# Kernel optimization log

Measured on AMD Instinct MI355X. Metric: run time of the kernel, lower is better.

Reference implementation:

```python
import jax, jax.numpy as jnp
import numpy as np

N_HEAD = 32
N_KV_HEAD = 8
HD = 64  # head dim
N_EMBD = 2048
B, T = 2, 2048
ROPE_THETA = 10000.0


def _apply_rope(x, cos, sin):
    # x: [B, T, H, HD]; cos/sin: [T, HD//2]. Interleaved complex pairs (even, odd),
    # matching torch.view_as_complex on x.reshape(..., -1, 2).
    x0 = x[..., 0::2]
    x1 = x[..., 1::2]
    c = cos[None, :, None, :]
    s = sin[None, :, None, :]
    o0 = x0 * c - x1 * s
    o1 = x0 * s + x1 * c
    return jnp.stack([o0, o1], axis=-1).reshape(x.shape)


def setup_inputs() -> dict:
    key = jax.random.key(0)
    k1, k2, k3 = jax.random.split(key, 3)
    x = jax.random.normal(k1, (B, T, N_EMBD), dtype=jnp.float32)
    Wqkv = jax.random.normal(k2, ((N_HEAD + 2 * N_KV_HEAD) * HD, N_EMBD), dtype=jnp.float32) * 0.02
    Wproj = jax.random.normal(k3, (N_EMBD, N_EMBD), dtype=jnp.float32) * 0.02
    # precompute_freqs_cis as in llm.c (llama path)
    freqs = 1.0 / (ROPE_THETA ** (np.arange(0, HD, 2, dtype=np.float32) / HD))
    ang = np.outer(np.arange(T, dtype=np.float32), freqs)  # [T, HD//2]
    freqs_cos = jnp.asarray(np.cos(ang), dtype=jnp.float32)
    freqs_sin = jnp.asarray(np.sin(ang), dtype=jnp.float32)
    return {"x": x, "Wqkv": Wqkv, "Wproj": Wproj,
            "freqs_cos": freqs_cos, "freqs_sin": freqs_sin, "start_pos": -1}


def reference(x, Wqkv, Wproj, freqs_cos, freqs_sin, start_pos):
    Bx, Tx, C = x.shape
    n_rep = N_HEAD // N_KV_HEAD
    qkv = x @ Wqkv.T  # [B, T, (H + 2*KV)*HD]
    q = qkv[..., : N_HEAD * HD].reshape(Bx, Tx, N_HEAD, HD)
    k = qkv[..., N_HEAD * HD: (N_HEAD + N_KV_HEAD) * HD].reshape(Bx, Tx, N_KV_HEAD, HD)
    v = qkv[..., (N_HEAD + N_KV_HEAD) * HD:].reshape(Bx, Tx, N_KV_HEAD, HD)
    # RoPE on q, k
    q = _apply_rope(q, freqs_cos, freqs_sin)
    k = _apply_rope(k, freqs_cos, freqs_sin)
    # start_pos < 0: training path, no KV cache. GQA repeat of kv heads.
    k = jnp.repeat(k, n_rep, axis=2)  # [B, T, H, HD]
    v = jnp.repeat(v, n_rep, axis=2)
    q = q.transpose(0, 2, 1, 3)  # [B, H, T, HD]
    k = k.transpose(0, 2, 1, 3)
    v = v.transpose(0, 2, 1, 3)
    scale = 1.0 / np.sqrt(HD).astype(np.float32)
    scores = jnp.einsum("bhtd,bhsd->bhts", q, k) * scale  # [B, H, T, T]
    causal = jnp.tril(jnp.ones((Tx, Tx), dtype=bool))
    scores = jnp.where(causal[None, None, :, :], scores, -jnp.inf)
    att = jax.nn.softmax(scores.astype(jnp.float32), axis=-1).astype(q.dtype)
    y = jnp.einsum("bhts,bhsd->bhtd", att, v)
    y = y.transpose(0, 2, 1, 3).reshape(Bx, Tx, C)
    return y @ Wproj.T
```

## Files before the change

kernel.cpp:

```cpp
#include <hip/hip_runtime.h>
#include <hip/hip_bf16.h>
#include <cstdint>

#define NH   32
#define NKV  8
#define HD   64
#define CE   2048
#define BB   2
#define TT   2048
#define QKVD 3072
#define MM   (BB*TT)

typedef float  f32x4  __attribute__((ext_vector_type(4)));
typedef float  f32x16 __attribute__((ext_vector_type(16)));
typedef short  s16x8  __attribute__((ext_vector_type(8)));
typedef unsigned short u16;

#define AS1 __attribute__((address_space(1)))
#define AS3 __attribute__((address_space(3)))
#define GLDS16(src, dst) __builtin_amdgcn_global_load_lds( \
    (const AS1 uint32_t*)(src), (AS3 uint32_t*)(dst), 16, 0, 0)

static __device__ __forceinline__ float bf2f(u16 u) {
    union { uint32_t u; float f; } v; v.u = ((uint32_t)u) << 16; return v.f;
}
static __device__ __forceinline__ u16 f2bf(float f) {
    union { float f; uint32_t u; } v; v.f = f;
    uint32_t r = v.u + 0x7fffu + ((v.u >> 16) & 1u);
    return (u16)(r >> 16);
}
static __device__ __forceinline__ uint32_t cvtpk(float lo, float hi) {
    uint32_t r;
    asm("v_cvt_pk_bf16_f32 %0, %1, %2" : "=v"(r) : "v"(lo), "v"(hi));
    return r;
}
static __device__ __forceinline__ void plswap(uint32_t &a, uint32_t &b) {
    asm volatile("v_permlane32_swap_b32 %0, %1" : "+v"(a), "+v"(b));
}

__global__ void k_f32_to_bf16(const float* __restrict__ in, uint32_t* __restrict__ out, int n8) {
    int i = blockIdx.x * blockDim.x + threadIdx.x;
    if (i >= n8) return;
    const float4* p = reinterpret_cast<const float4*>(in) + (size_t)i * 2;
    float4 a = p[0], b = p[1];
    uint4 o;
    o.x = cvtpk(a.x, a.y); o.y = cvtpk(a.z, a.w);
    o.z = cvtpk(b.x, b.y); o.w = cvtpk(b.z, b.w);
    *reinterpret_cast<uint4*>(out + (size_t)i * 4) = o;
}

__global__ __launch_bounds__(256) void k_gemm_qkv(const u16* __restrict__ A,
                                                  const u16* __restrict__ Bm,
                                                  u16* __restrict__ Qb,
                                                  u16* __restrict__ Kb,
                                                  u16* __restrict__ Vt,
                                                  const float* __restrict__ fcos,
                                                  const float* __restrict__ fsin) {
    __shared__ u16 As[128 * 32];
    __shared__ u16 Bs[128 * 32];
    const int K = CE;
    const int c  = blockIdx.x + 24 * blockIdx.y;
    const int nc = (c & 7) * 96 + (c >> 3);
    const int m0 = (nc / 24) * 128;
    const int n0 = (nc % 24) * 128;

    const int tid  = threadIdx.x;
    const int w    = tid >> 6;
    const int lane = tid & 63;
    const int lr   = lane & 15, lg = lane >> 4;
    const int wm   = (w >> 1) * 64, wn = (w & 1) * 64;

    const int o0 = w * 2048 + lane * 16, o1 = o0 + 1024;
    const int ar0 = o0 >> 6, ar1 = o1 >> 6;
    const int ac0 = (o0 & 63) >> 1, ac1 = (o1 & 63) >> 1;
    const size_t aof0 = (size_t)(m0 + ar0) * K + ac0;
    const size_t aof1 = (size_t)(m0 + ar1) * K + ac1;
    const size_t bof0 = (size_t)(n0 + ar0) * K + ac0;
    const size_t bof1 = (size_t)(n0 + ar1) * K + ac1;
    u16* dA0 = &As[w * 1024];       u16* dA1 = &As[w * 1024 + 512];
    u16* dB0 = &Bs[w * 1024];       u16* dB1 = &Bs[w * 1024 + 512];

    f32x4 acc[4][4] = {};

    for (int k0 = 0; k0 < K; k0 += 32) {
        GLDS16(A  + aof0 + k0, dA0);
        GLDS16(A  + aof1 + k0, dA1);
        GLDS16(Bm + bof0 + k0, dB0);
        GLDS16(Bm + bof1 + k0, dB1);
        __syncthreads();
        s16x8 af[4], bf[4];
        #pragma unroll
        for (int i = 0; i < 4; ++i)
            af[i] = *reinterpret_cast<const s16x8*>(&As[(wm + i * 16 + lr) * 32 + lg * 8]);
        #pragma unroll
        for (int j = 0; j < 4; ++j)
            bf[j] = *reinterpret_cast<const s16x8*>(&Bs[(wn + j * 16 + lr) * 32 + lg * 8]);
        #pragma unroll
        for (int i = 0; i < 4; ++i)
            #pragma unroll
            for (int j = 0; j < 4; ++j)
                acc[i][j] = __builtin_amdgcn_mfma_f32_16x16x32_bf16(af[i], bf[j], acc[i][j], 0, 0, 0);
        __syncthreads();
    }

    const float QS = 0.18033688011112042f;
    const int bb = m0 / TT;
    const int tb = m0 - bb * TT + wm;
    #pragma unroll
    for (int i = 0; i < 4; ++i) {
        const int t0 = tb + i * 16 + lg * 4;
        #pragma unroll
        for (int j = 0; j < 4; ++j) {
            const int n = n0 + wn + j * 16 + lr;
            if (n0 < NH * HD) {
                const int hh = n >> 6, d = n & 63;
                #pragma unroll
                for (int r = 0; r < 4; ++r) {
                    const int t = t0 + r;
                    const float cc = fcos[t * 32 + (d >> 1)];
                    const float ss = fsin[t * 32 + (d >> 1)];
                    float v = acc[i][j][r];
                    float p = __shfl_xor(v, 1, 64);
                    float o = ((lr & 1) ? (p * ss + v * cc) : (v * cc - p * ss)) * QS;
                    float po = __shfl_xor(o, 1, 64);
                    if (!(lr & 1))
                        *reinterpret_cast<uint32_t*>(Qb + ((size_t)((bb * NH + hh) * TT + t)) * HD + d) = cvtpk(o, po);
                }
            } else if (n0 < (NH + NKV) * HD) {
                const int fk = n - NH * HD;
                const int hh = fk >> 6, d = fk & 63;
                #pragma unroll
                for (int r = 0; r < 4; ++r) {
                    const int t = t0 + r;
                    const float cc = fcos[t * 32 + (d >> 1)];
                    const float ss = fsin[t * 32 + (d >> 1)];
                    float v = acc[i][j][r];
                    float p = __shfl_xor(v, 1, 64);
                    float o = (lr & 1) ? (p * ss + v * cc) : (v * cc - p * ss);
                    float po = __shfl_xor(o, 1, 64);
                    if (!(lr & 1))
                        *reinterpret_cast<uint32_t*>(Kb + ((size_t)((bb * NKV + hh) * TT + t)) * HD + d) = cvtpk(o, po);
                }
            } else {
                const int fv = n - (NH + NKV) * HD;
                const int vh = fv >> 6, d = fv & 63;
                uint2 st;
                st.x = cvtpk(acc[i][j][0], acc[i][j][1]);
                st.y = cvtpk(acc[i][j][2], acc[i][j][3]);
                *reinterpret_cast<uint2*>(Vt + ((size_t)(bb * NKV + vh) * HD + d) * TT + t0) = st;
            }
        }
    }
}

__global__ __launch_bounds__(256) void k_gemm_bt(const u16* __restrict__ A,
                                                 const u16* __restrict__ Bm,
                                                 float* __restrict__ Cout,
                                                 int M, int N, int K) {
    __shared__ u16 As[128 * 32];
    __shared__ u16 Bs[128 * 32];
    const int c  = blockIdx.x + 16 * blockIdx.y;
    const int nc = (c & 7) * 64 + (c >> 3);
    const int m0 = (nc >> 4) * 128;
    const int n0 = (nc & 15) * 128;

    const int tid  = threadIdx.x;
    const int w    = tid >> 6;
    const int lane = tid & 63;
    const int lr   = lane & 15, lg = lane >> 4;
    const int wm   = (w >> 1) * 64, wn = (w & 1) * 64;

    const int o0 = w * 2048 + lane * 16, o1 = o0 + 1024;
    const int ar0 = o0 >> 6, ar1 = o1 >> 6;
    const int ac0 = (o0 & 63) >> 1, ac1 = (o1 & 63) >> 1;
    const size_t aof0 = (size_t)(m0 + ar0) * K + ac0;
    const size_t aof1 = (size_t)(m0 + ar1) * K + ac1;
    const size_t bof0 = (size_t)(n0 + ar0) * K + ac0;
    const size_t bof1 = (size_t)(n0 + ar1) * K + ac1;
    u16* dA0 = &As[w * 1024];       u16* dA1 = &As[w * 1024 + 512];
    u16* dB0 = &Bs[w * 1024];       u16* dB1 = &Bs[w * 1024 + 512];

    f32x4 acc[4][4] = {};

    for (int k0 = 0; k0 < K; k0 += 32) {
        GLDS16(A  + aof0 + k0, dA0);
        GLDS16(A  + aof1 + k0, dA1);
        GLDS16(Bm + bof0 + k0, dB0);
        GLDS16(Bm + bof1 + k0, dB1);
        __syncthreads();
        s16x8 af[4], bf[4];
        #pragma unroll
        for (int i = 0; i < 4; ++i)
            af[i] = *reinterpret_cast<const s16x8*>(&As[(wm + i * 16 + lr) * 32 + lg * 8]);
        #pragma unroll
        for (int j = 0; j < 4; ++j)
            bf[j] = *reinterpret_cast<const s16x8*>(&Bs[(wn + j * 16 + lr) * 32 + lg * 8]);
        #pragma unroll
        for (int i = 0; i < 4; ++i)
            #pragma unroll
            for (int j = 0; j < 4; ++j)
                acc[i][j] = __builtin_amdgcn_mfma_f32_16x16x32_bf16(af[i], bf[j], acc[i][j], 0, 0, 0);
        __syncthreads();
    }

    #pragma unroll
    for (int i = 0; i < 4; ++i)
        #pragma unroll
        for (int j = 0; j < 4; ++j)
            #pragma unroll
            for (int r = 0; r < 4; ++r) {
                int m = m0 + wm + i * 16 + lg * 4 + r;
                int n = n0 + wn + j * 16 + lr;
                Cout[(size_t)m * N + n] = acc[i][j][r];
            }
}

__global__ __launch_bounds__(512) void k_attn(const u16* __restrict__ Q,
                                              const u16* __restrict__ Kb,
                                              const u16* __restrict__ Vt,
                                              u16* __restrict__ Y) {
    __shared__ u16 Ks[2][4096];
    __shared__ u16 Vs[2][4096];

    const int tid = threadIdx.x;
    const int w = tid >> 6, lane = tid & 63;
    const int wv = w & 3, half = w >> 2;
    const int ql = lane & 31, hi = lane >> 5;
    const int hi16 = hi << 4;
    const int b = blockIdx.z, h = blockIdx.y, kvh = h >> 2;
    const int u = blockIdx.x;

    const int j1 = b ? (8 + u) : (15 - u);
    const int j2 = b ? (7 - u) : u;
    const int jq = half ? j2 : j1;
    const int q0w  = jq * 128 + wv * 32;
    const int nt   = 2 * j1 + 2;
    const int tmxw = (q0w + 31) >> 6;
    const int qabs = q0w + ql;

    const u16* qbase = Q  + ((size_t)(b * NH  + h  ) * TT) * HD;
    const u16* kbase = Kb + ((size_t)(b * NKV + kvh) * TT) * HD;
    const u16* vbase = Vt + ((size_t)(b * NKV + kvh) * HD) * TT;

    const int o0 = w * 1024 + lane * 16;
    const int r0 = o0 >> 7;
    const int c0 = (o0 & 127) ^ ((r0 & 7) << 4);
    const size_t kof0 = (size_t)r0 * HD + (c0 >> 1);
    const size_t vof0 = (size_t)r0 * TT + (c0 >> 1);

    const char* KsB = (const char*)&Ks[0][0];
    const char* VsB = (const char*)&Vs[0][0];
    const int krb0 = (0 * 32 + ql) * 128, ksz0 = ((0 * 32 + ql) & 7) << 4;
    const int krb1 = (1 * 32 + ql) * 128, ksz1 = ((1 * 32 + ql) & 7) << 4;

    s16x8 qf[4];
    #pragma unroll
    for (int ds = 0; ds < 4; ++ds)
        qf[ds] = *reinterpret_cast<const s16x8*>(qbase + (size_t)qabs * HD + ds * 16 + 8 * hi);
    asm volatile("s_waitcnt vmcnt(0)" ::: "memory");

    GLDS16(kbase + kof0, &Ks[0][w * 512]);
    GLDS16(vbase + vof0, &Vs[0][w * 512]);

    float mrow = -1e30f, lrowp = 0.f;
    f32x16 oT0 = {}, oT1 = {};

    for (int t = 0; t < nt; ++t) {
        const int cur = t & 1;
        const int kv0 = t * 64;
        if (t + 1 < nt) {
            GLDS16(kbase + (size_t)(kv0 + 64) * HD + kof0, &Ks[cur ^ 1][w * 512]);
            GLDS16(vbase + (kv0 + 64) + vof0, &Vs[cur ^ 1][w * 512]);
            asm volatile("s_waitcnt vmcnt(2)" ::: "memory");
        } else {
            asm volatile("s_waitcnt vmcnt(0)" ::: "memory");
        }
        __builtin_amdgcn_s_barrier();
        __builtin_amdgcn_sched_barrier(0);

        if (t <= tmxw) {
            const int bufo = cur * 8192;

            f32x16 sc0 = {}, sc1 = {};
            __builtin_amdgcn_s_setprio(1);
            #pragma unroll
            for (int ds = 0; ds < 4; ++ds) {
                s16x8 k0 = *reinterpret_cast<const s16x8*>(KsB + bufo + krb0 + (((ds << 5) | hi16) ^ ksz0));
                s16x8 k1 = *reinterpret_cast<const s16x8*>(KsB + bufo + krb1 + (((ds << 5) | hi16) ^ ksz1));
                sc0 = __builtin_amdgcn_mfma_f32_32x32x16_bf16(k0, qf[ds], sc0, 0, 0, 0);
                sc1 = __builtin_amdgcn_mfma_f32_32x32x16_bf16(k1, qf[ds], sc1, 0, 0, 0);
            }
            __builtin_amdgcn_s_setprio(0);

            float p0[16], p1[16];
            #pragma unroll
            for (int r = 0; r < 16; ++r) { p0[r] = sc0[r]; p1[r] = sc1[r]; }

            if (t == tmxw) {
                const int dq = qabs - kv0 - 4 * hi;
                #pragma unroll
                for (int r = 0; r < 16; ++r) {
                    const int kr = (r & 3) + 8 * (r >> 2);
                    p0[r] = (kr      <= dq) ? p0[r] : -1e30f;
                    p1[r] = (kr + 32 <= dq) ? p1[r] : -1e30f;
                }
            }

            float tmax = fmaxf(p0[0], p1[0]);
            #pragma unroll
            for (int r = 1; r < 16; ++r) tmax = fmaxf(fmaxf(tmax, p0[r]), p1[r]);
            if (__any(tmax > mrow + 8.f)) {
                float tf = fmaxf(tmax, __shfl_xor(tmax, 32, 64));
                float mn = fmaxf(mrow, tf);
                float alpha = __builtin_amdgcn_exp2f(mrow - mn);
                mrow = mn;
                lrowp *= alpha;
                #pragma unroll
                for (int r = 0; r < 16; ++r) { oT0[r] *= alpha; oT1[r] *= alpha; }
            }

            float sum = 0.f;
            #pragma unroll
            for (int r = 0; r < 16; ++r) {
                p0[r] = __builtin_amdgcn_exp2f(p0[r] - mrow);
                p1[r] = __builtin_amdgcn_exp2f(p1[r] - mrow);
                sum += p0[r] + p1[r];
            }
            lrowp += sum;

            __builtin_amdgcn_s_setprio(1);
            #pragma unroll
            for (int ks = 0; ks < 2; ++ks) {
                uint32_t a0 = cvtpk(p0[ks * 8 + 0], p0[ks * 8 + 1]);
                uint32_t b0 = cvtpk(p0[ks * 8 + 4], p0[ks * 8 + 5]);
                plswap(a0, b0);
                uint32_t a1 = cvtpk(p0[ks * 8 + 2], p0[ks * 8 + 3]);
                uint32_t b1 = cvtpk(p0[ks * 8 + 6], p0[ks * 8 + 7]);
                plswap(a1, b1);
                union { uint32_t d[4]; s16x8 v; } pb;
                pb.d[0] = a0; pb.d[1] = a1; pb.d[2] = b0; pb.d[3] = b1;
                const int colb = (0 << 6) | (ks << 5) | hi16;
                s16x8 v0 = *reinterpret_cast<const s16x8*>(VsB + bufo + krb0 + (colb ^ ksz0));
                s16x8 v1 = *reinterpret_cast<const s16x8*>(VsB + bufo + krb1 + (colb ^ ksz1));
                oT0 = __builtin_amdgcn_mfma_f32_32x32x16_bf16(v0, pb.v, oT0, 0, 0, 0);
                oT1 = __builtin_amdgcn_mfma_f32_32x32x16_bf16(v1, pb.v, oT1, 0, 0, 0);
            }
            #pragma unroll
            for (int ks = 0; ks < 2; ++ks) {
                uint32_t a0 = cvtpk(p1[ks * 8 + 0], p1[ks * 8 + 1]);
                uint32_t b0 = cvtpk(p1[ks * 8 + 4], p1[ks * 8 + 5]);
                plswap(a0, b0);
                uint32_t a1 = cvtpk(p1[ks * 8 + 2], p1[ks * 8 + 3]);
                uint32_t b1 = cvtpk(p1[ks * 8 + 6], p1[ks * 8 + 7]);
                plswap(a1, b1);
                union { uint32_t d[4]; s16x8 v; } pb;
                pb.d[0] = a0; pb.d[1] = a1; pb.d[2] = b0; pb.d[3] = b1;
                const int colb = (1 << 6) | (ks << 5) | hi16;
                s16x8 v0 = *reinterpret_cast<const s16x8*>(VsB + bufo + krb0 + (colb ^ ksz0));
                s16x8 v1 = *reinterpret_cast<const s16x8*>(VsB + bufo + krb1 + (colb ^ ksz1));
                oT0 = __builtin_amdgcn_mfma_f32_32x32x16_bf16(v0, pb.v, oT0, 0, 0, 0);
                oT1 = __builtin_amdgcn_mfma_f32_32x32x16_bf16(v1, pb.v, oT1, 0, 0, 0);
            }
            __builtin_amdgcn_s_setprio(0);
        }

        __builtin_amdgcn_sched_barrier(0);
        __builtin_amdgcn_s_barrier();
    }

    lrowp += __shfl_xor(lrowp, 32, 64);
    const float rinv = 1.f / lrowp;
    const size_t yrow = ((size_t)(b * TT + qabs) * NH + h) * HD;
    #pragma unroll
    for (int rp = 0; rp < 8; ++rp) {
        const int d = ((2 * rp) & 3) + 8 * (rp >> 1) + 4 * hi;
        *reinterpret_cast<uint32_t*>(Y + yrow + d) =
            cvtpk(oT0[2 * rp] * rinv, oT0[2 * rp + 1] * rinv);
        *reinterpret_cast<uint32_t*>(Y + yrow + 32 + d) =
            cvtpk(oT1[2 * rp] * rinv, oT1[2 * rp + 1] * rinv);
    }
}

extern "C" void kernel_launch(void* const* d_in, const int* in_sizes, int n_in,
                              void* d_out, int out_size, void* d_ws, size_t ws_size,
                              hipStream_t stream) {
    (void)in_sizes; (void)n_in; (void)out_size; (void)ws_size;
    const float* x     = (const float*)d_in[0];
    const float* wqkv  = (const float*)d_in[1];
    const float* wproj = (const float*)d_in[2];
    const float* fcos  = (const float*)d_in[3];
    const float* fsin  = (const float*)d_in[4];

    char* ws = (char*)d_ws;
    size_t off = 0;
    auto alloc = [&](size_t bytes) { void* p = ws + off; off += (bytes + 255) & ~(size_t)255; return p; };
    u16* Xbf  = (u16*)alloc((size_t)MM * CE * 2);
    u16* Wqb  = (u16*)alloc((size_t)QKVD * CE * 2);
    u16* Wpb  = (u16*)alloc((size_t)CE * CE * 2);
    u16* Qb   = (u16*)alloc((size_t)BB * NH * TT * HD * 2);
    u16* Kbuf = (u16*)alloc((size_t)BB * NKV * TT * HD * 2);
    u16* Vtb  = (u16*)alloc((size_t)BB * NKV * HD * TT * 2);
    u16* Yb   = (u16*)alloc((size_t)MM * CE * 2);

    k_f32_to_bf16<<<(MM * CE / 8 + 255) / 256, 256, 0, stream>>>(x, (uint32_t*)Xbf, MM * CE / 8);
    k_f32_to_bf16<<<(QKVD * CE / 8 + 255) / 256, 256, 0, stream>>>(wqkv, (uint32_t*)Wqb, QKVD * CE / 8);
    k_f32_to_bf16<<<(CE * CE / 8 + 255) / 256, 256, 0, stream>>>(wproj, (uint32_t*)Wpb, CE * CE / 8);

    dim3 g1(QKVD / 128, MM / 128);
    k_gemm_qkv<<<g1, 256, 0, stream>>>(Xbf, Wqb, Qb, Kbuf, Vtb, fcos, fsin);

    dim3 ga(8, NH, BB);
    k_attn<<<ga, 512, 0, stream>>>(Qb, Kbuf, Vtb, Yb);

    dim3 g2(CE / 128, MM / 128);
    k_gemm_bt<<<g2, 256, 0, stream>>>(Yb, Wpb, (float*)d_out, MM, CE, CE);
}
```

Measured before the change: 206.6 us.

## Fuse conversion kernels, interleave RoPE tables, nontemporal output stores, rebalance attention tiles

```diff
diff --git a/kernel.cpp b/kernel.cpp
--- a/kernel.cpp
+++ b/kernel.cpp
@@ -38,15 +38,38 @@
     asm volatile("v_permlane32_swap_b32 %0, %1" : "+v"(a), "+v"(b));
 }
 
-__global__ void k_f32_to_bf16(const float* __restrict__ in, uint32_t* __restrict__ out, int n8) {
-    int i = blockIdx.x * blockDim.x + threadIdx.x;
-    if (i >= n8) return;
-    const float4* p = reinterpret_cast<const float4*>(in) + (size_t)i * 2;
+static __device__ __forceinline__ void cvt8(const float* __restrict__ in, uint32_t* __restrict__ out) {
+    const float4* p = reinterpret_cast<const float4*>(in);
     float4 a = p[0], b = p[1];
     uint4 o;
     o.x = cvtpk(a.x, a.y); o.y = cvtpk(a.z, a.w);
     o.z = cvtpk(b.x, b.y); o.w = cvtpk(b.z, b.w);
-    *reinterpret_cast<uint4*>(out + (size_t)i * 4) = o;
+    *reinterpret_cast<uint4*>(out) = o;
+}
+__global__ void k_cvt_all(const float* __restrict__ x, const float* __restrict__ wqkv,
+                          const float* __restrict__ wproj,
+                          uint32_t* __restrict__ xo, uint32_t* __restrict__ wqo,
+                          uint32_t* __restrict__ wpo,
+                          const float* __restrict__ fcos, const float* __restrict__ fsin,
+                          float2* __restrict__ csT) {
+    const int n1 = MM * CE / 8, n2 = QKVD * CE / 8, n3 = CE * CE / 8, n4 = 32 * TT / 8;
+    int i = blockIdx.x * blockDim.x + threadIdx.x;
+    if (i < n1) {
+        cvt8(x + (size_t)i * 8, xo + (size_t)i * 4);
+    } else if (i < n1 + n2) {
+        int k = i - n1;
+        cvt8(wqkv + (size_t)k * 8, wqo + (size_t)k * 4);
+    } else if (i < n1 + n2 + n3) {
+        int k = i - n1 - n2;
+        cvt8(wproj + (size_t)k * 8, wpo + (size_t)k * 4);
+    } else if (i < n1 + n2 + n3 + n4) {
+        int k = (i - n1 - n2 - n3) * 8;
+        #pragma unroll
+        for (int jj = 0; jj < 8; ++jj) {
+            float2 cs; cs.x = fcos[k + jj]; cs.y = fsin[k + jj];
+            csT[k + jj] = cs;
+        }
+    }
 }
 
 __global__ __launch_bounds__(256) void k_gemm_qkv(const u16* __restrict__ A,
@@ -54,8 +77,7 @@
                                                   u16* __restrict__ Qb,
                                                   u16* __restrict__ Kb,
                                                   u16* __restrict__ Vt,
-                                                  const float* __restrict__ fcos,
-                                                  const float* __restrict__ fsin) {
+                                                  const float2* __restrict__ csT) {
     __shared__ u16 As[128 * 32];
     __shared__ u16 Bs[128 * 32];
     const int K = CE;
@@ -117,11 +139,10 @@
                 #pragma unroll
                 for (int r = 0; r < 4; ++r) {
                     const int t = t0 + r;
-                    const float cc = fcos[t * 32 + (d >> 1)];
-                    const float ss = fsin[t * 32 + (d >> 1)];
+                    const float2 cs = csT[t * 32 + (d >> 1)];
                     float v = acc[i][j][r];
                     float p = __shfl_xor(v, 1, 64);
-                    float o = ((lr & 1) ? (p * ss + v * cc) : (v * cc - p * ss)) * QS;
+                    float o = ((lr & 1) ? (p * cs.y + v * cs.x) : (v * cs.x - p * cs.y)) * QS;
                     float po = __shfl_xor(o, 1, 64);
                     if (!(lr & 1))
                         *reinterpret_cast<uint32_t*>(Qb + ((size_t)((bb * NH + hh) * TT + t)) * HD + d) = cvtpk(o, po);
@@ -132,11 +153,10 @@
                 #pragma unroll
                 for (int r = 0; r < 4; ++r) {
                     const int t = t0 + r;
-                    const float cc = fcos[t * 32 + (d >> 1)];
-                    const float ss = fsin[t * 32 + (d >> 1)];
+                    const float2 cs = csT[t * 32 + (d >> 1)];
                     float v = acc[i][j][r];
                     float p = __shfl_xor(v, 1, 64);
-                    float o = (lr & 1) ? (p * ss + v * cc) : (v * cc - p * ss);
+                    float o = (lr & 1) ? (p * cs.y + v * cs.x) : (v * cs.x - p * cs.y);
                     float po = __shfl_xor(o, 1, 64);
                     if (!(lr & 1))
                         *reinterpret_cast<uint32_t*>(Kb + ((size_t)((bb * NKV + hh) * TT + t)) * HD + d) = cvtpk(o, po);
@@ -211,7 +231,7 @@
             for (int r = 0; r < 4; ++r) {
                 int m = m0 + wm + i * 16 + lg * 4 + r;
                 int n = n0 + wn + j * 16 + lr;
-                Cout[(size_t)m * N + n] = acc[i][j][r];
+                __builtin_nontemporal_store(acc[i][j][r], &Cout[(size_t)m * N + n]);
             }
 }
 
@@ -230,8 +250,8 @@
     const int b = blockIdx.z, h = blockIdx.y, kvh = h >> 2;
     const int u = blockIdx.x;
 
-    const int j1 = b ? (8 + u) : (15 - u);
-    const int j2 = b ? (7 - u) : u;
+    const int m  = b ? (7 - u) : u;
+    const int j1 = 2 * m + 1, j2 = 2 * m;
     const int jq = half ? j2 : j1;
     const int q0w  = jq * 128 + wv * 32;
     const int nt   = 2 * j1 + 2;
@@ -394,20 +414,22 @@
     char* ws = (char*)d_ws;
     size_t off = 0;
     auto alloc = [&](size_t bytes) { void* p = ws + off; off += (bytes + 255) & ~(size_t)255; return p; };
-    u16* Xbf  = (u16*)alloc((size_t)MM * CE * 2);
-    u16* Wqb  = (u16*)alloc((size_t)QKVD * CE * 2);
-    u16* Wpb  = (u16*)alloc((size_t)CE * CE * 2);
-    u16* Qb   = (u16*)alloc((size_t)BB * NH * TT * HD * 2);
-    u16* Kbuf = (u16*)alloc((size_t)BB * NKV * TT * HD * 2);
-    u16* Vtb  = (u16*)alloc((size_t)BB * NKV * HD * TT * 2);
-    u16* Yb   = (u16*)alloc((size_t)MM * CE * 2);
-
-    k_f32_to_bf16<<<(MM * CE / 8 + 255) / 256, 256, 0, stream>>>(x, (uint32_t*)Xbf, MM * CE / 8);
-    k_f32_to_bf16<<<(QKVD * CE / 8 + 255) / 256, 256, 0, stream>>>(wqkv, (uint32_t*)Wqb, QKVD * CE / 8);
-    k_f32_to_bf16<<<(CE * CE / 8 + 255) / 256, 256, 0, stream>>>(wproj, (uint32_t*)Wpb, CE * CE / 8);
+    u16*    Xbf  = (u16*)alloc((size_t)MM * CE * 2);
+    u16*    Wqb  = (u16*)alloc((size_t)QKVD * CE * 2);
+    u16*    Wpb  = (u16*)alloc((size_t)CE * CE * 2);
+    u16*    Qb   = (u16*)alloc((size_t)BB * NH * TT * HD * 2);
+    u16*    Kbuf = (u16*)alloc((size_t)BB * NKV * TT * HD * 2);
+    u16*    Vtb  = (u16*)alloc((size_t)BB * NKV * HD * TT * 2);
+    u16*    Yb   = (u16*)alloc((size_t)MM * CE * 2);
+    float2* csT  = (float2*)alloc((size_t)32 * TT * sizeof(float2));
+
+    const int ncvt = MM * CE / 8 + QKVD * CE / 8 + CE * CE / 8 + 32 * TT / 8;
+    k_cvt_all<<<(ncvt + 255) / 256, 256, 0, stream>>>(x, wqkv, wproj,
+                                                      (uint32_t*)Xbf, (uint32_t*)Wqb, (uint32_t*)Wpb,
+                                                      fcos, fsin, csT);
 
     dim3 g1(QKVD / 128, MM / 128);
-    k_gemm_qkv<<<g1, 256, 0, stream>>>(Xbf, Wqb, Qb, Kbuf, Vtb, fcos, fsin);
+    k_gemm_qkv<<<g1, 256, 0, stream>>>(Xbf, Wqb, Qb, Kbuf, Vtb, csT);
 
     dim3 ga(8, NH, BB);
     k_attn<<<ga, 512, 0, stream>>>(Qb, Kbuf, Vtb, Yb);
```

Result: no change. 207.9 us (+0.6%).
